# Optimization experiments

Measured on AMD Instinct MI355X. Metric: run time of the kernel, lower is better.

## Reference

```python
import jax, jax.numpy as jnp
import numpy as np
from jax import lax

TAU_SYN = 0.5
TAU_MEM_MIN, TAU_MEM_MAX = 0.8, 0.98
VTH_MIN, VTH_MAX = 0.05, 0.5
ALPHA = 4.0  # surrogate sharpness (forward output unaffected)

B, T, N = 32, 128, 4096


def setup_inputs() -> dict:
    key = jax.random.key(0)
    k1, k2, k3 = jax.random.split(key, 3)
    x = jax.random.normal(k1, (B, T, N), dtype=jnp.float32)
    # learnable per-neuron decay / threshold, initialized inside their clamp ranges
    tau_mem = TAU_MEM_MIN + (TAU_MEM_MAX - TAU_MEM_MIN) * jax.random.uniform(k2, (N,), dtype=jnp.float32)
    v_threshold = VTH_MIN + (VTH_MAX - VTH_MIN) * jax.random.uniform(k3, (N,), dtype=jnp.float32)
    return {"x": x, "tau_mem": tau_mem, "v_threshold": v_threshold}


def _lin_scan(a, b):
    """Parallel scan of y[t] = a[t]*y[t-1] + b[t] along axis 1 (y[-1]=0)."""
    def combine(c1, c2):
        a1, b1 = c1
        a2, b2 = c2
        return a1 * a2, a2 * b1 + b2
    _, y = lax.associative_scan(combine, (a, b), axis=1)
    return y


def reference(x, tau_mem, v_threshold):
    tau_m = jnp.clip(tau_mem, TAU_MEM_MIN, TAU_MEM_MAX)          # (N,)
    thr = jnp.clip(v_threshold, VTH_MIN, VTH_MAX)                # (N,)
    # synaptic current: i_syn[t] = tau_syn * i_syn[t-1] + x[t]
    a_syn = jnp.full_like(x, TAU_SYN)
    i_syn = _lin_scan(a_syn, x)                                  # (B,T,N)
    # membrane: v[t] = tau_mem * v[t-1] + (1 - tau_mem) * i_syn[t]
    a_mem = jnp.broadcast_to(tau_m, x.shape)
    v_mem = _lin_scan(a_mem, (1.0 - tau_m) * i_syn)              # (B,T,N)
    # hard binary spikes (Heaviside at per-neuron threshold)
    spikes = (v_mem >= thr).astype(x.dtype)                      # (B,T,N)
    return spikes
```

## Files before the change

kernel.cpp:

```cpp
#include <hip/hip_runtime.h>

constexpr int B = 32;
constexpr int T = 128;
constexpr int N = 4096;

__global__ __launch_bounds__(256) void lif_scan_kernel(
    const float* __restrict__ x,
    const float* __restrict__ tau_mem,
    const float* __restrict__ v_th,
    float* __restrict__ out)
{
    const int tid = blockIdx.x * blockDim.x + threadIdx.x;
    const int nh  = N / 2;
    const int b   = tid / nh;
    const int n2  = (tid - b * nh) * 2;

    float2 tm = *reinterpret_cast<const float2*>(tau_mem + n2);
    float2 tv = *reinterpret_cast<const float2*>(v_th + n2);

    const float tmf0 = fminf(fmaxf(tm.x, 0.8f), 0.98f);
    const float tmf1 = fminf(fmaxf(tm.y, 0.8f), 0.98f);
    const float thf0 = fminf(fmaxf(tv.x, 0.05f), 0.5f);
    const float thf1 = fminf(fmaxf(tv.y, 0.05f), 0.5f);

    const double t0 = (double)tmf0, t1 = (double)tmf1;
    const double c0 = 1.0 - t0,     c1 = 1.0 - t1;
    const double h0 = (double)thf0, h1 = (double)thf1;

    const size_t base = (size_t)b * T * N + (size_t)n2;
    const float* xp = x + base;
    float*       op = out + base;

    double is0 = 0.0, is1 = 0.0, v0 = 0.0, v1 = 0.0;

#pragma unroll 8
    for (int t = 0; t < T; ++t) {
        const float2 xv = *reinterpret_cast<const float2*>(xp + (size_t)t * N);
        is0 = fma(0.5, is0, (double)xv.x);
        is1 = fma(0.5, is1, (double)xv.y);
        v0 = fma(t0, v0, c0 * is0);
        v1 = fma(t1, v1, c1 * is1);
        float2 s;
        s.x = (v0 >= h0) ? 1.0f : 0.0f;
        s.y = (v1 >= h1) ? 1.0f : 0.0f;
        *reinterpret_cast<float2*>(op + (size_t)t * N) = s;
    }
}

extern "C" void kernel_launch(void* const* d_in, const int* in_sizes, int n_in,
                              void* d_out, int out_size, void* d_ws, size_t ws_size,
                              hipStream_t stream) {
    const float* x       = (const float*)d_in[0];
    const float* tau_mem = (const float*)d_in[1];
    const float* v_th    = (const float*)d_in[2];
    float* out           = (float*)d_out;

    const int threads = B * (N / 2);
    dim3 block(256);
    dim3 grid(threads / 256);
    lif_scan_kernel<<<grid, block, 0, stream>>>(x, tau_mem, v_th, out);
}
```

Baseline: 116.7 us.

## Use one neuron per thread with register double-buffered nontemporal loads

Each thread now handles a single neuron instead of two, which doubles the thread count to B*N. The time loop is split into groups of 8 steps, and the next group's inputs are prefetched into registers while the current group is computed. Loads and stores use nontemporal builtins so the streamed data avoids polluting the cache. This aims to keep more memory requests in flight on a bandwidth-bound scan, at the cost of scalar rather than float2 accesses and more registers per thread for the buffers.

```diff
diff --git a/kernel.cpp b/kernel.cpp
--- a/kernel.cpp
+++ b/kernel.cpp
@@ -3,6 +3,8 @@
 constexpr int B = 32;
 constexpr int T = 128;
 constexpr int N = 4096;
+constexpr int UNR = 8;
+constexpr int NG = T / UNR;
 
 __global__ __launch_bounds__(256) void lif_scan_kernel(
     const float* __restrict__ x,
@@ -11,39 +13,47 @@
     float* __restrict__ out)
 {
     const int tid = blockIdx.x * blockDim.x + threadIdx.x;
-    const int nh  = N / 2;
-    const int b   = tid / nh;
-    const int n2  = (tid - b * nh) * 2;
+    const int b   = tid >> 12;
+    const int n   = tid & (N - 1);
 
-    float2 tm = *reinterpret_cast<const float2*>(tau_mem + n2);
-    float2 tv = *reinterpret_cast<const float2*>(v_th + n2);
+    const float tmf = fminf(fmaxf(tau_mem[n], 0.8f), 0.98f);
+    const float thf = fminf(fmaxf(v_th[n],  0.05f), 0.5f);
 
-    const float tmf0 = fminf(fmaxf(tm.x, 0.8f), 0.98f);
-    const float tmf1 = fminf(fmaxf(tm.y, 0.8f), 0.98f);
-    const float thf0 = fminf(fmaxf(tv.x, 0.05f), 0.5f);
-    const float thf1 = fminf(fmaxf(tv.y, 0.05f), 0.5f);
+    const double tm = (double)tmf;
+    const double cm = 1.0 - tm;
+    const double th = (double)thf;
 
-    const double t0 = (double)tmf0, t1 = (double)tmf1;
-    const double c0 = 1.0 - t0,     c1 = 1.0 - t1;
-    const double h0 = (double)thf0, h1 = (double)thf1;
-
-    const size_t base = (size_t)b * T * N + (size_t)n2;
+    const size_t base = (size_t)b * T * N + (size_t)n;
     const float* xp = x + base;
     float*       op = out + base;
 
-    double is0 = 0.0, is1 = 0.0, v0 = 0.0, v1 = 0.0;
+    double is = 0.0, v = 0.0;
 
-#pragma unroll 8
-    for (int t = 0; t < T; ++t) {
-        const float2 xv = *reinterpret_cast<const float2*>(xp + (size_t)t * N);
-        is0 = fma(0.5, is0, (double)xv.x);
-        is1 = fma(0.5, is1, (double)xv.y);
-        v0 = fma(t0, v0, c0 * is0);
-        v1 = fma(t1, v1, c1 * is1);
-        float2 s;
-        s.x = (v0 >= h0) ? 1.0f : 0.0f;
-        s.y = (v1 >= h1) ? 1.0f : 0.0f;
-        *reinterpret_cast<float2*>(op + (size_t)t * N) = s;
+    float buf[UNR];
+#pragma unroll
+    for (int u = 0; u < UNR; ++u)
+        buf[u] = __builtin_nontemporal_load(xp + (size_t)u * N);
+
+    for (int g = 0; g < NG; ++g) {
+        float nbuf[UNR];
+        if (g + 1 < NG) {
+            const float* xg = xp + (size_t)(g + 1) * UNR * N;
+#pragma unroll
+            for (int u = 0; u < UNR; ++u)
+                nbuf[u] = __builtin_nontemporal_load(xg + (size_t)u * N);
+        }
+
+        float* og = op + (size_t)g * UNR * N;
+#pragma unroll
+        for (int u = 0; u < UNR; ++u) {
+            is = fma(0.5, is, (double)buf[u]);
+            v = fma(tm, v, cm * is);
+            __builtin_nontemporal_store((v >= th) ? 1.0f : 0.0f,
+                                        og + (size_t)u * N);
+        }
+
+#pragma unroll
+        for (int u = 0; u < UNR; ++u) buf[u] = nbuf[u];
     }
 }
 
@@ -55,7 +65,7 @@
     const float* v_th    = (const float*)d_in[2];
     float* out           = (float*)d_out;
 
-    const int threads = B * (N / 2);
+    const int threads = B * N;
     dim3 block(256);
     dim3 grid(threads / 256);
     lif_scan_kernel<<<grid, block, 0, stream>>>(x, tau_mem, v_th, out);
```

Result: slower. 124.3 us (+6.5%).
